# Performance work log

Measured on AMD Instinct MI355X. Metric: run time of the kernel, lower is better.

The kernel has to match this reference:

```python
import jax, jax.numpy as jnp
import numpy as np

N, C, HI, WI = 8, 3, 512, 512   # src_img NCHW (input_img_size)
HO, WO = 2048, 2048             # output canvas (output_img_size[2:])
EPS = 1e-8


def _transform_one(img, coor_row):
    """Replicates: sigmoid box params -> theta -> F.affine_grid -> F.grid_sample
    (bilinear, zeros padding, align_corners=False). Theta has zero off-diagonals,
    so the grid is separable in x/y and the bilinear sample factorizes.
    img: [C, HI, WI]; coor_row: [4]. Returns (sample [C,HO,WO], mask [HO,WO])."""
    x = jax.nn.sigmoid(coor_row[0]) * WO
    y = jax.nn.sigmoid(coor_row[1]) * HO
    w = jax.nn.sigmoid(coor_row[2]) * WO
    h = jax.nn.sigmoid(coor_row[3]) * HO
    a = WO / (w + EPS)
    tx = 2.0 / WO * (WO / 2.0 - x) * a
    b = HO / (h + EPS)
    ty = 2.0 / HO * (HO / 2.0 - y) * b
    # affine_grid base coords (align_corners=False): center-of-pixel normalized
    xs = (2.0 * jnp.arange(WO, dtype=img.dtype) + 1.0) / WO - 1.0
    ys = (2.0 * jnp.arange(HO, dtype=img.dtype) + 1.0) / HO - 1.0
    gx = a * xs + tx          # [WO]
    gy = b * ys + ty          # [HO]
    # grid_sample unnormalize (align_corners=False)
    ix = ((gx + 1.0) * WI - 1.0) / 2.0
    iy = ((gy + 1.0) * HI - 1.0) / 2.0
    x0f = jnp.floor(ix); y0f = jnp.floor(iy)
    wx1 = ix - x0f; wx0 = 1.0 - wx1
    wy1 = iy - y0f; wy0 = 1.0 - wy1
    x0 = x0f.astype(jnp.int32); x1 = x0 + 1
    y0 = y0f.astype(jnp.int32); y1 = y0 + 1
    vx0 = ((x0 >= 0) & (x0 < WI)).astype(img.dtype)
    vx1 = ((x1 >= 0) & (x1 < WI)).astype(img.dtype)
    vy0 = ((y0 >= 0) & (y0 < HI)).astype(img.dtype)
    vy1 = ((y1 >= 0) & (y1 < HI)).astype(img.dtype)
    x0c = jnp.clip(x0, 0, WI - 1); x1c = jnp.clip(x1, 0, WI - 1)
    y0c = jnp.clip(y0, 0, HI - 1); y1c = jnp.clip(y1, 0, HI - 1)
    wyv0 = wy0 * vy0; wyv1 = wy1 * vy1
    wxv0 = wx0 * vx0; wxv1 = wx1 * vx1
    # separable bilinear gather with zero padding
    rows = img[:, y0c, :] * wyv0[None, :, None] + img[:, y1c, :] * wyv1[None, :, None]  # [C,HO,WI]
    samp = rows[:, :, x0c] * wxv0[None, None, :] + rows[:, :, x1c] * wxv1[None, None, :]  # [C,HO,WO]
    # grid_sample of an all-ones mask == sum of in-bounds bilinear weights (separable)
    mask = (wyv0 + wyv1)[:, None] * (wxv0 + wxv1)[None, :]  # [HO,WO]
    return samp, mask


def _composite(src_img, bg_img, coor):
    def step(bg, inp):
        img, c = inp
        s, m = _transform_one(img, c)
        bg = bg * (1.0 - m)[None, None] + (s * m[None])[None]
        return bg, None
    bg, _ = jax.lax.scan(step, bg_img, (src_img, coor))
    return bg


def setup_inputs() -> dict:
    key = jax.random.key(0)
    k1, k2, k3 = jax.random.split(key, 3)
    src_img = jax.random.normal(k1, (N, C, HI, WI), dtype=jnp.float32)
    bg_img = jax.random.uniform(k2, (1, C, HO, WO), dtype=jnp.float32)
    coor = jax.random.normal(k3, (N, 4), dtype=jnp.float32)  # nn.Parameter
    return {"src_img": src_img, "bg_img": bg_img, "coor": coor}


def reference(src_img, bg_img, coor):
    return _composite(src_img, bg_img, coor)
```

## Files before the change

kernel.cpp:

```cpp
#include <hip/hip_runtime.h>

#define WI 512
#define HI 512
#define WO 2048
#define HO 2048
#define NIMG 8
#define CCH 3
#define EPS 1e-8f
#define PLANE (HI * WI)

__device__ __forceinline__ void ycalc(const float4 P, const float ys,
                                      float& wyv0, float& wyv1,
                                      int& y0o, int& y1o) {
    const float gy  = P.z * ys + P.w;
    const float iy  = ((gy + 1.0f) * (float)HI - 1.0f) * 0.5f;
    const float y0f = floorf(iy);
    const float fy1 = iy - y0f;
    const float fy0 = 1.0f - fy1;
    const float y1f = y0f + 1.0f;
    const float v0  = (y0f >= 0.0f && y0f < (float)HI) ? 1.0f : 0.0f;
    const float v1  = (y1f >= 0.0f && y1f < (float)HI) ? 1.0f : 0.0f;
    wyv0 = fy0 * v0;
    wyv1 = fy1 * v1;
    y0o = (int)fminf(fmaxf(y0f, 0.0f), (float)(HI - 1)) * WI;
    y1o = (int)fminf(fmaxf(y1f, 0.0f), (float)(HI - 1)) * WI;
}

__device__ __forceinline__ void stage_rows(float (*dst)[WI],
                                           const float* __restrict__ src,
                                           const int n,
                                           const float wyv0, const float wyv1,
                                           const int y0o, const int y1o,
                                           const int tid) {
    if (tid < 128) {
        const int x = tid << 2;
        const float* base = src + n * (CCH * PLANE);
#pragma unroll
        for (int c = 0; c < CCH; c++) {
            const float4 r0 = *(const float4*)(base + c * PLANE + y0o + x);
            const float4 r1 = *(const float4*)(base + c * PLANE + y1o + x);
            float4 rc;
            rc.x = r0.x * wyv0 + r1.x * wyv1;
            rc.y = r0.y * wyv0 + r1.y * wyv1;
            rc.z = r0.z * wyv0 + r1.z * wyv1;
            rc.w = r0.w * wyv0 + r1.w * wyv1;
            *(float4*)&dst[c][x] = rc;
        }
    }
}

__launch_bounds__(256)
__global__ void diffcomp_fused(const float* __restrict__ src,
                               const float* __restrict__ bg,
                               const float* __restrict__ coor,
                               float* __restrict__ out) {
    __shared__ float  cs[2][CCH][WI];
    __shared__ float4 prm[NIMG];

    const int tid = threadIdx.x;
    const int ho  = (int)((blockIdx.x * 997u) & 2047u);

    if (tid < NIMG) {
        const float cx = coor[tid * 4 + 0];
        const float cy = coor[tid * 4 + 1];
        const float cw = coor[tid * 4 + 2];
        const float chh = coor[tid * 4 + 3];
        const float x = (1.0f / (1.0f + expf(-cx))) * (float)WO;
        const float y = (1.0f / (1.0f + expf(-cy))) * (float)HO;
        const float w = (1.0f / (1.0f + expf(-cw))) * (float)WO;
        const float h = (1.0f / (1.0f + expf(-chh))) * (float)HO;
        const float a  = (float)WO / (w + EPS);
        const float tx = (2.0f / (float)WO) * ((float)WO * 0.5f - x) * a;
        const float b  = (float)HO / (h + EPS);
        const float ty = (2.0f / (float)HO) * ((float)HO * 0.5f - y) * b;
        prm[tid] = make_float4(a, tx, b, ty);
    }
    __syncthreads();

    const float ys = (2.0f * (float)ho + 1.0f) / (float)HO - 1.0f;

    unsigned cov = 0u;
#pragma unroll
    for (int n = 0; n < NIMG; n++) {
        float w0, w1; int a0, a1;
        ycalc(prm[n], ys, w0, w1, a0, a1);
        if (w0 + w1 > 0.0f) cov |= (1u << n);
    }

    const int rowbase = ho * WO + (tid << 3);
    float acc[CCH][8];
#pragma unroll
    for (int c = 0; c < CCH; c++) {
        const float4 b0 = *(const float4*)(bg + c * HO * WO + rowbase);
        const float4 b1 = *(const float4*)(bg + c * HO * WO + rowbase + 4);
        acc[c][0] = b0.x; acc[c][1] = b0.y; acc[c][2] = b0.z; acc[c][3] = b0.w;
        acc[c][4] = b1.x; acc[c][5] = b1.y; acc[c][6] = b1.z; acc[c][7] = b1.w;
    }

    if (cov) {
        int cur = (int)__builtin_ctz(cov);
        unsigned rest = cov & (cov - 1u);

        float4 Pc = prm[cur];
        float w0c, w1c; int y0c, y1c;
        ycalc(Pc, ys, w0c, w1c, y0c, y1c);
        float myc = w0c + w1c;
        stage_rows(cs[0], src, cur, w0c, w1c, y0c, y1c, tid);
        __syncthreads();

        int s = 0;
        while (true) {
            const int nxt = rest ? (int)__builtin_ctz(rest) : -1;
            float4 Pn; float mynxt = 0.0f;
            if (nxt >= 0) {
                Pn = prm[nxt];
                float w0n, w1n; int a0, a1;
                ycalc(Pn, ys, w0n, w1n, a0, a1);
                mynxt = w0n + w1n;
                stage_rows(cs[s ^ 1], src, nxt, w0n, w1n, a0, a1, tid);
            }

            const float a  = Pc.x;
            const float tx = Pc.y;
#pragma unroll
            for (int p = 0; p < 8; p++) {
                const int wo = (tid << 3) + p;
                const float xs  = (2.0f * (float)wo + 1.0f) / (float)WO - 1.0f;
                const float gx  = a * xs + tx;
                const float ix  = ((gx + 1.0f) * (float)WI - 1.0f) * 0.5f;
                const float x0f = floorf(ix);
                const float fx1 = ix - x0f;
                const float fx0 = 1.0f - fx1;
                const float vx0 = (x0f >= 0.0f && x0f < (float)WI) ? 1.0f : 0.0f;
                const float vx1 = (x0f >= -1.0f && x0f < (float)(WI - 1)) ? 1.0f : 0.0f;
                const float wxv0 = fx0 * vx0;
                const float wxv1 = fx1 * vx1;
                const int bse = (int)fminf(fmaxf(x0f, 0.0f), (float)(WI - 2));
                const int x0i = (int)fminf(fmaxf(x0f, 0.0f), (float)(WI - 1));
                const int x1i = (int)fminf(fmaxf(x0f + 1.0f, 0.0f), (float)(WI - 1));
                const bool hi0 = (x0i != bse);
                const bool hi1 = (x1i != bse);
                const float m  = myc * (wxv0 + wxv1);
                const float om = 1.0f - m;
#pragma unroll
                for (int c = 0; c < CCH; c++) {
                    const float qa = cs[s][c][bse];
                    const float qb = cs[s][c][bse + 1];
                    const float v0 = hi0 ? qb : qa;
                    const float v1 = hi1 ? qb : qa;
                    const float sc = v0 * wxv0 + v1 * wxv1;
                    acc[c][p] = acc[c][p] * om + sc * m;
                }
            }

            __syncthreads();
            if (nxt < 0) break;
            Pc = Pn; myc = mynxt;
            rest &= rest - 1u;
            s ^= 1;
        }
    }

#pragma unroll
    for (int c = 0; c < CCH; c++) {
        const float4 o0 = make_float4(acc[c][0], acc[c][1], acc[c][2], acc[c][3]);
        const float4 o1 = make_float4(acc[c][4], acc[c][5], acc[c][6], acc[c][7]);
        *(float4*)(out + c * HO * WO + rowbase)     = o0;
        *(float4*)(out + c * HO * WO + rowbase + 4) = o1;
    }
}

extern "C" void kernel_launch(void* const* d_in, const int* in_sizes, int n_in,
                              void* d_out, int out_size, void* d_ws, size_t ws_size,
                              hipStream_t stream) {
    const float* src  = (const float*)d_in[0];
    const float* bg   = (const float*)d_in[1];
    const float* coor = (const float*)d_in[2];
    float* out = (float*)d_out;
    (void)d_ws; (void)ws_size;

    hipLaunchKernelGGL(diffcomp_fused, dim3(HO), dim3(256), 0, stream,
                       src, bg, coor, out);
}
```

Baseline: 134.5 us.

## Split rows into 512-pixel segments and stage only the needed source span

Result: slower. 151.6 us (+12.8%).

```diff
diff --git a/kernel.cpp b/kernel.cpp
--- a/kernel.cpp
+++ b/kernel.cpp
@@ -9,9 +9,19 @@
 #define EPS 1e-8f
 #define PLANE (HI * WI)
 
-__device__ __forceinline__ void ycalc(const float4 P, const float ys,
-                                      float& wyv0, float& wyv1,
-                                      int& y0o, int& y1o) {
+#define SEG  512
+#define TPB  128
+#define PXT  4
+#define MAXR 516
+
+struct ImgUni {
+    float wy0, wy1, my;
+    int   y0o, y1o;
+    int   t0, t1;
+};
+
+__device__ __forceinline__ bool img_uniforms(const float4 P, const float ys,
+                                             const int wo0, ImgUni& u) {
     const float gy  = P.z * ys + P.w;
     const float iy  = ((gy + 1.0f) * (float)HI - 1.0f) * 0.5f;
     const float y0f = floorf(iy);
@@ -20,50 +30,41 @@
     const float y1f = y0f + 1.0f;
     const float v0  = (y0f >= 0.0f && y0f < (float)HI) ? 1.0f : 0.0f;
     const float v1  = (y1f >= 0.0f && y1f < (float)HI) ? 1.0f : 0.0f;
-    wyv0 = fy0 * v0;
-    wyv1 = fy1 * v1;
-    y0o = (int)fminf(fmaxf(y0f, 0.0f), (float)(HI - 1)) * WI;
-    y1o = (int)fminf(fmaxf(y1f, 0.0f), (float)(HI - 1)) * WI;
+    u.wy0 = fy0 * v0;
+    u.wy1 = fy1 * v1;
+    u.my  = u.wy0 + u.wy1;
+    u.y0o = (int)fminf(fmaxf(y0f, 0.0f), (float)(HI - 1)) * WI;
+    u.y1o = (int)fminf(fmaxf(y1f, 0.0f), (float)(HI - 1)) * WI;
+    if (!(u.my > 0.0f)) return false;
+
+    const float a  = P.x, tx = P.y;
+    const float xsf = (2.0f * (float)wo0 + 1.0f) / (float)WO - 1.0f;
+    const float xsl = (2.0f * (float)(wo0 + SEG - 1) + 1.0f) / (float)WO - 1.0f;
+    const float ixf = ((a * xsf + tx + 1.0f) * (float)WI - 1.0f) * 0.5f;
+    const float ixl = ((a * xsl + tx + 1.0f) * (float)WI - 1.0f) * 0.5f;
+    if (ixl <= -1.0f || ixf >= (float)WI) return false;
+    u.t0 = (int)fminf(fmaxf(floorf(ixf), 0.0f), (float)(WI - 1));
+    u.t1 = (int)fminf(fmaxf(floorf(ixl) + 1.0f, 0.0f), (float)(WI - 1));
+    return true;
 }
 
-__device__ __forceinline__ void stage_rows(float (*dst)[WI],
-                                           const float* __restrict__ src,
-                                           const int n,
-                                           const float wyv0, const float wyv1,
-                                           const int y0o, const int y1o,
-                                           const int tid) {
-    if (tid < 128) {
-        const int x = tid << 2;
-        const float* base = src + n * (CCH * PLANE);
-#pragma unroll
-        for (int c = 0; c < CCH; c++) {
-            const float4 r0 = *(const float4*)(base + c * PLANE + y0o + x);
-            const float4 r1 = *(const float4*)(base + c * PLANE + y1o + x);
-            float4 rc;
-            rc.x = r0.x * wyv0 + r1.x * wyv1;
-            rc.y = r0.y * wyv0 + r1.y * wyv1;
-            rc.z = r0.z * wyv0 + r1.z * wyv1;
-            rc.w = r0.w * wyv0 + r1.w * wyv1;
-            *(float4*)&dst[c][x] = rc;
-        }
-    }
-}
-
-__launch_bounds__(256)
-__global__ void diffcomp_fused(const float* __restrict__ src,
-                               const float* __restrict__ bg,
-                               const float* __restrict__ coor,
-                               float* __restrict__ out) {
-    __shared__ float  cs[2][CCH][WI];
+__launch_bounds__(TPB)
+__global__ void diffcomp_fused7(const float* __restrict__ src,
+                                const float* __restrict__ bg,
+                                const float* __restrict__ coor,
+                                float* __restrict__ out) {
+    __shared__ float  cs[2][CCH][MAXR];
     __shared__ float4 prm[NIMG];
 
     const int tid = threadIdx.x;
-    const int ho  = (int)((blockIdx.x * 997u) & 2047u);
+    const int b   = blockIdx.x;
+    const int row = b >> 2;
+    const int wo0 = (b & 3) * SEG;
 
     if (tid < NIMG) {
-        const float cx = coor[tid * 4 + 0];
-        const float cy = coor[tid * 4 + 1];
-        const float cw = coor[tid * 4 + 2];
+        const float cx  = coor[tid * 4 + 0];
+        const float cy  = coor[tid * 4 + 1];
+        const float cw  = coor[tid * 4 + 2];
         const float chh = coor[tid * 4 + 3];
         const float x = (1.0f / (1.0f + expf(-cx))) * (float)WO;
         const float y = (1.0f / (1.0f + expf(-cy))) * (float)HO;
@@ -71,103 +72,105 @@
         const float h = (1.0f / (1.0f + expf(-chh))) * (float)HO;
         const float a  = (float)WO / (w + EPS);
         const float tx = (2.0f / (float)WO) * ((float)WO * 0.5f - x) * a;
-        const float b  = (float)HO / (h + EPS);
-        const float ty = (2.0f / (float)HO) * ((float)HO * 0.5f - y) * b;
-        prm[tid] = make_float4(a, tx, b, ty);
+        const float bb = (float)HO / (h + EPS);
+        const float ty = (2.0f / (float)HO) * ((float)HO * 0.5f - y) * bb;
+        prm[tid] = make_float4(a, tx, bb, ty);
     }
     __syncthreads();
 
-    const float ys = (2.0f * (float)ho + 1.0f) / (float)HO - 1.0f;
+    const float ys = (2.0f * (float)row + 1.0f) / (float)HO - 1.0f;
 
     unsigned cov = 0u;
 #pragma unroll
     for (int n = 0; n < NIMG; n++) {
-        float w0, w1; int a0, a1;
-        ycalc(prm[n], ys, w0, w1, a0, a1);
-        if (w0 + w1 > 0.0f) cov |= (1u << n);
+        ImgUni u;
+        if (img_uniforms(prm[n], ys, wo0, u)) cov |= (1u << n);
     }
 
-    const int rowbase = ho * WO + (tid << 3);
-    float acc[CCH][8];
+    const int base = row * WO + wo0 + tid;
+    float acc[CCH][PXT];
 #pragma unroll
-    for (int c = 0; c < CCH; c++) {
-        const float4 b0 = *(const float4*)(bg + c * HO * WO + rowbase);
-        const float4 b1 = *(const float4*)(bg + c * HO * WO + rowbase + 4);
-        acc[c][0] = b0.x; acc[c][1] = b0.y; acc[c][2] = b0.z; acc[c][3] = b0.w;
-        acc[c][4] = b1.x; acc[c][5] = b1.y; acc[c][6] = b1.z; acc[c][7] = b1.w;
-    }
+    for (int c = 0; c < CCH; c++)
+#pragma unroll
+        for (int p = 0; p < PXT; p++)
+            acc[c][p] = bg[c * HO * WO + base + p * TPB];
 
     if (cov) {
-        int cur = (int)__builtin_ctz(cov);
-        unsigned rest = cov & (cov - 1u);
+        auto stage = [&](int slot, int n) {
+            ImgUni u;
+            img_uniforms(prm[n], ys, wo0, u);
+            const float* ib = src + n * (CCH * PLANE);
+            const int R = u.t1 - u.t0 + 1;
+            for (int i = tid; i < R; i += TPB) {
+#pragma unroll
+                for (int c = 0; c < CCH; c++) {
+                    const float r0 = ib[c * PLANE + u.y0o + u.t0 + i];
+                    const float r1 = ib[c * PLANE + u.y1o + u.t0 + i];
+                    cs[slot][c][i] = r0 * u.wy0 + r1 * u.wy1;
+                }
+            }
+        };
 
-        float4 Pc = prm[cur];
-        float w0c, w1c; int y0c, y1c;
-        ycalc(Pc, ys, w0c, w1c, y0c, y1c);
-        float myc = w0c + w1c;
-        stage_rows(cs[0], src, cur, w0c, w1c, y0c, y1c, tid);
-        __syncthreads();
-
-        int s = 0;
-        while (true) {
-            const int nxt = rest ? (int)__builtin_ctz(rest) : -1;
-            float4 Pn; float mynxt = 0.0f;
-            if (nxt >= 0) {
-                Pn = prm[nxt];
-                float w0n, w1n; int a0, a1;
-                ycalc(Pn, ys, w0n, w1n, a0, a1);
-                mynxt = w0n + w1n;
-                stage_rows(cs[s ^ 1], src, nxt, w0n, w1n, a0, a1, tid);
-            }
-
-            const float a  = Pc.x;
-            const float tx = Pc.y;
+        auto blend = [&](int slot, int n) {
+            ImgUni u;
+            img_uniforms(prm[n], ys, wo0, u);
+            const float a  = prm[n].x;
+            const float tx = prm[n].y;
+            const int lim = u.t1 - u.t0;
 #pragma unroll
-            for (int p = 0; p < 8; p++) {
-                const int wo = (tid << 3) + p;
+            for (int p = 0; p < PXT; p++) {
+                const int wo = wo0 + p * TPB + tid;
                 const float xs  = (2.0f * (float)wo + 1.0f) / (float)WO - 1.0f;
                 const float gx  = a * xs + tx;
                 const float ix  = ((gx + 1.0f) * (float)WI - 1.0f) * 0.5f;
                 const float x0f = floorf(ix);
                 const float fx1 = ix - x0f;
                 const float fx0 = 1.0f - fx1;
-                const float vx0 = (x0f >= 0.0f && x0f < (float)WI) ? 1.0f : 0.0f;
-                const float vx1 = (x0f >= -1.0f && x0f < (float)(WI - 1)) ? 1.0f : 0.0f;
-                const float wxv0 = fx0 * vx0;
-                const float wxv1 = fx1 * vx1;
-                const int bse = (int)fminf(fmaxf(x0f, 0.0f), (float)(WI - 2));
-                const int x0i = (int)fminf(fmaxf(x0f, 0.0f), (float)(WI - 1));
-                const int x1i = (int)fminf(fmaxf(x0f + 1.0f, 0.0f), (float)(WI - 1));
-                const bool hi0 = (x0i != bse);
-                const bool hi1 = (x1i != bse);
-                const float m  = myc * (wxv0 + wxv1);
+                const float x1f = x0f + 1.0f;
+                const float v0  = (x0f >= 0.0f && x0f < (float)WI) ? 1.0f : 0.0f;
+                const float v1  = (x1f >= 0.0f && x1f < (float)WI) ? 1.0f : 0.0f;
+                const float wx0 = fx0 * v0;
+                const float wx1 = fx1 * v1;
+                int x0r = (int)fminf(fmaxf(x0f, 0.0f), (float)(WI - 1)) - u.t0;
+                int x1r = (int)fminf(fmaxf(x1f, 0.0f), (float)(WI - 1)) - u.t0;
+                x0r = min(max(x0r, 0), lim);
+                x1r = min(max(x1r, 0), lim);
+                const float m  = u.my * (wx0 + wx1);
                 const float om = 1.0f - m;
 #pragma unroll
                 for (int c = 0; c < CCH; c++) {
-                    const float qa = cs[s][c][bse];
-                    const float qb = cs[s][c][bse + 1];
-                    const float v0 = hi0 ? qb : qa;
-                    const float v1 = hi1 ? qb : qa;
-                    const float sc = v0 * wxv0 + v1 * wxv1;
+                    const float q0 = cs[slot][c][x0r];
+                    const float q1 = cs[slot][c][x1r];
+                    const float sc = q0 * wx0 + q1 * wx1;
                     acc[c][p] = acc[c][p] * om + sc * m;
                 }
             }
+        };
 
+        int cur = (int)__builtin_ctz(cov);
+        unsigned rest = cov & (cov - 1u);
+
+        stage(0, cur);
+        __syncthreads();
+
+        int s = 0;
+        while (true) {
+            const int nxt = rest ? (int)__builtin_ctz(rest) : -1;
+            if (nxt >= 0) stage(s ^ 1, nxt);
+            blend(s, cur);
             __syncthreads();
             if (nxt < 0) break;
-            Pc = Pn; myc = mynxt;
+            cur = nxt;
             rest &= rest - 1u;
             s ^= 1;
         }
     }
 
 #pragma unroll
-    for (int c = 0; c < CCH; c++) {
-        const float4 o0 = make_float4(acc[c][0], acc[c][1], acc[c][2], acc[c][3]);
-        const float4 o1 = make_float4(acc[c][4], acc[c][5], acc[c][6], acc[c][7]);
-        *(float4*)(out + c * HO * WO + rowbase)     = o0;
-        *(float4*)(out + c * HO * WO + rowbase + 4) = o1;
-    }
+    for (int c = 0; c < CCH; c++)
+#pragma unroll
+        for (int p = 0; p < PXT; p++)
+            out[c * HO * WO + base + p * TPB] = acc[c][p];
 }
 
 extern "C" void kernel_launch(void* const* d_in, const int* in_sizes, int n_in,
@@ -179,6 +182,6 @@
     float* out = (float*)d_out;
     (void)d_ws; (void)ws_size;
 
-    hipLaunchKernelGGL(diffcomp_fused, dim3(HO), dim3(256), 0, stream,
+    hipLaunchKernelGGL(diffcomp_fused7, dim3(HO * 4), dim3(TPB), 0, stream,
                        src, bg, coor, out);
 }
```
